# Performance work log

Measured on AMD Instinct MI355X. Metric: run time of the kernel, lower is better.

Reference implementation:

```python
import jax, jax.numpy as jnp
import numpy as np

IN_FEATURES = 256
OUT_FEATURES = 256
GRID_SIZE = 5
SPLINE_ORDER = 3
GRID_LO, GRID_HI = -1.0, 1.0


def _basis_matrix(spline_order):
    # Uniform B-spline basis matrix, replicating calculate_basis_matrix.
    M = np.array([[1.0]], dtype=np.float32)
    scalar = 1.0
    for k in range(2, spline_order + 2):
        t1 = np.pad(M, ((0, 1), (0, 0)))
        t3 = np.pad(M, ((1, 0), (0, 0)))
        t2 = np.zeros((k - 1, k), np.float32)
        t4 = np.zeros((k - 1, k), np.float32)
        for i in range(k - 1):
            t2[i, i] = i + 1
            t2[i, i + 1] = k - (i + 2)
            t4[i, i] = -1.0
            t4[i, i + 1] = 1.0
        M = t1 @ t2 + t3 @ t4
        scalar *= 1.0 / (k - 1)
    return (M * scalar).astype(np.float32)


def setup_inputs() -> dict:
    key = jax.random.key(0)
    kx, kw = jax.random.split(key)
    x = jax.random.uniform(kx, (16384, IN_FEATURES), dtype=jnp.float32)  # in [0,1) within grid range
    weight = jax.random.normal(kw, (IN_FEATURES, OUT_FEATURES, GRID_SIZE + SPLINE_ORDER + 1), dtype=jnp.float32)
    return {"x": x, "weight": weight}


def reference(x, weight):
    s, g = SPLINE_ORDER, GRID_SIZE
    h = (GRID_HI - GRID_LO) / g
    # grid: [-s..g+s] * h + lo, length g + 2s + 1
    grid1d = jnp.arange(-s, g + s + 1, dtype=jnp.float32) * h + GRID_LO

    xi = x[..., None]  # [N, in, 1]
    intervals = (xi >= grid1d[:-1]) & (xi < grid1d[1:])  # [N, in, g+2s]
    idx = jnp.argmax(intervals, axis=-1)  # first true; 0 if none

    # power bases u = [1, u1, u1^2, ..., u1^s]
    floor_val = idx.astype(x.dtype) * h + GRID_LO
    u1 = (x - floor_val) / h  # [N, in]
    u = jnp.stack([jnp.ones_like(u1), u1] + [u1 ** i for i in range(2, s + 1)], axis=-1)  # [N, in, s+1]

    # basis-matrix slice indices (argmax over [zeros | intervals])
    idx2 = jnp.where(intervals.any(-1), idx + 1, 0)  # [N, in]
    floor_idx = (2 * s + g + 1) - idx2  # [N, in]

    B = jnp.asarray(_basis_matrix(s))  # [s+1, s+1]
    B_pad = jnp.pad(B, ((0, 0), (s + g, s + g)))  # [s+1, (s+1)+2(s+g)]
    cols = floor_idx[..., None] + jnp.arange(s + g)  # [N, in, s+g]
    gathered = B_pad[:, cols]  # [s+1, N, in, s+g]

    basis_out = jnp.einsum('nip,pniq->niq', u, gathered)  # [N, in, s+g]
    basis_out = jnp.nan_to_num(basis_out)

    spline_w = weight[:, :, :-1]  # [in, out, s+g]
    base_w = weight[:, :, -1]     # [in, out]
    y = jnp.einsum('niq,ioq->no', basis_out, spline_w) + jnp.einsum('ni,io->no', jax.nn.silu(x), base_w)
    return y
```

## Files before the change

### kernel.cpp

```cpp
#include <hip/hip_runtime.h>
#include <hip/hip_bf16.h>


#define M_TOTAL 16384
#define IF 256
#define OF 256
#define NKT 32
#define THREADS 512

typedef __attribute__((ext_vector_type(8))) __bf16 bf16x8;
typedef __attribute__((ext_vector_type(4))) float f32x4;

__global__ void repack_w(const float* __restrict__ w, __bf16* __restrict__ img) {
    int g = blockIdx.x * 256 + threadIdx.x;
    int lane = g & 63, frag = g >> 6;
    int n  = frag & 3;
    int cg = (frag >> 2) & 3;
    int ks = (frag >> 4) & 1;
    int kt = frag >> 5;
    int col = cg * 64 + n * 16 + (lane & 15);
    int i   = kt * 8 + ks * 4 + (lane >> 4);
    const float s6 = 1.0f / 6.0f;
    bf16x8 v;
#pragma unroll
    for (int c = 0; c < 8; ++c) {
        float f = (c < 6) ? w[(size_t)i * 2304 + col * 9 + c + 2] * s6
                : (c == 6) ? w[(size_t)i * 2304 + col * 9 + 8] : 0.0f;
        v[c] = (__bf16)f;
    }
    ((bf16x8*)img)[g] = v;
}

__device__ __forceinline__ bf16x8 phi_pack(float x) {
    float t  = fmaf(x, 2.5f, 5.5f);
    float fi = floorf(t);
    float u  = (t - fi) - 3.0f;
    float u2 = u * u, u3 = u2 * u;
    float w0 = fmaf(-1.f, u3, fmaf( 3.f, u2, fmaf(-3.f, u, 1.f)));
    float w1 = fmaf( 3.f, u3, fmaf(-6.f, u2, 4.f));
    float w2 = fmaf(-3.f, u3, fmaf( 3.f, u2, fmaf( 3.f, u, 1.f)));
    float w3 = u3;
    bool e1 = fi > 5.5f;
    bool e2 = fi > 6.5f;
    float v0 = e1 ? 0.f : w0;
    float v1 = e2 ? 0.f : (e1 ? w0 : w1);
    float v2 = e2 ? w0  : (e1 ? w1 : w2);
    float v3 = e2 ? w1  : (e1 ? w2 : w3);
    float v4 = e2 ? w2  : (e1 ? w3 : 0.f);
    float v5 = e2 ? w3  : 0.f;
    float sl = x * __builtin_amdgcn_rcpf(1.f + __expf(-x));
    bf16x8 v;
    v[0] = (__bf16)v0; v[1] = (__bf16)v1; v[2] = (__bf16)v2; v[3] = (__bf16)v3;
    v[4] = (__bf16)v4; v[5] = (__bf16)v5; v[6] = (__bf16)sl; v[7] = (__bf16)0.f;
    return v;
}

__device__ __forceinline__ bf16x8 gather_frag(const float* __restrict__ W,
                                              int kt, int col, int ks, int lane) {
    int c2 = col + (lane & 15);
    int i  = kt * 8 + ks * 4 + (lane >> 4);
    const float s6 = 1.0f / 6.0f;
    bf16x8 v;
#pragma unroll
    for (int c = 0; c < 8; ++c) {
        float f = (c < 6) ? W[(size_t)i * 2304 + c2 * 9 + c + 2] * s6
                : (c == 6) ? W[(size_t)i * 2304 + c2 * 9 + 8] : 0.0f;
        v[c] = (__bf16)f;
    }
    return v;
}

template <bool DIRECT_B>
__global__ __launch_bounds__(THREADS, 2)
void kan_gemm(const float* __restrict__ X, const __bf16* __restrict__ Bimg,
              const float* __restrict__ W, float* __restrict__ Y) {
    __shared__ alignas(16) char lds[65536];

    const int tid  = threadIdx.x;
    const int lane = tid & 63;
    const int wv   = tid >> 6;
    const int cg   = wv & 3;
    const int rowg = wv >> 2;
    const int l15  = lane & 15;
    const int l4   = lane >> 4;
    const int brow0 = blockIdx.x * 64;

    const int prow = tid >> 3;
    const int pi   = tid & 7;
    const int pr7  = prow & 7;
    const float* xrow = X + (size_t)(brow0 + prow) * IF;
    const int awbase = prow * 512;

    const int sw    = l15 & 7;
    const int arow0 = rowg * 32 + l15;

    const char* ib = (const char*)Bimg + cg * 4096 + lane * 16;

    f32x4 acc[2][4] = {};
    bf16x8 breg[2][8];
    float xs[4];

#pragma unroll
    for (int w = 0; w < 4; ++w) xs[w] = xrow[w * 8 + pi];
    if (!DIRECT_B) {
#pragma unroll
        for (int ks = 0; ks < 2; ++ks)
#pragma unroll
            for (int n = 0; n < 4; ++n)
                breg[0][ks * 4 + n] = *(const bf16x8*)(ib + ks * 16384 + n * 1024);
    } else {
#pragma unroll
        for (int ks = 0; ks < 2; ++ks)
#pragma unroll
            for (int n = 0; n < 4; ++n)
                breg[0][ks * 4 + n] = gather_frag(W, 0, cg * 64 + n * 16, ks, lane);
    }
#pragma unroll
    for (int w = 0; w < 4; ++w)
        *(bf16x8*)(lds + awbase + (((w * 8 + pi) ^ pr7) << 4)) = phi_pack(xs[w]);
#pragma unroll
    for (int w = 0; w < 4; ++w) xs[w] = xrow[32 + w * 8 + pi];
    __syncthreads();

    for (int c = 0; c < 8; ++c) {
        const char* Ar = lds + ((c & 1) << 15);
        char* Aw = lds + (((c + 1) & 1) << 15);

#pragma unroll
        for (int ktl = 0; ktl < 4; ++ktl) {
            const int kt  = c * 4 + ktl;
            const int ktn = (kt < NKT - 1) ? kt + 1 : kt;

            if (!DIRECT_B) {
                const char* p = ib + (size_t)ktn * 32768;
#pragma unroll
                for (int ks = 0; ks < 2; ++ks)
#pragma unroll
                    for (int n = 0; n < 4; ++n)
                        breg[(ktl + 1) & 1][ks * 4 + n]
                            = *(const bf16x8*)(p + ks * 16384 + n * 1024);
            } else {
#pragma unroll
                for (int ks = 0; ks < 2; ++ks)
#pragma unroll
                    for (int n = 0; n < 4; ++n)
                        breg[(ktl + 1) & 1][ks * 4 + n]
                            = gather_frag(W, ktn, cg * 64 + n * 16, ks, lane);
            }

            bf16x8 aF[2][2];
#pragma unroll
            for (int m = 0; m < 2; ++m)
#pragma unroll
                for (int ks = 0; ks < 2; ++ks)
                    aF[m][ks] = *(const bf16x8*)(Ar + (arow0 + m * 16) * 512
                                    + (((ktl * 8 + ks * 4 + l4) ^ sw) << 4));

            __builtin_amdgcn_s_setprio(1);
#pragma unroll
            for (int ks = 0; ks < 2; ++ks)
#pragma unroll
                for (int m = 0; m < 2; ++m)
#pragma unroll
                    for (int n = 0; n < 4; ++n)
                        acc[m][n] = __builtin_amdgcn_mfma_f32_16x16x32_bf16(
                            aF[m][ks], breg[ktl & 1][ks * 4 + n], acc[m][n], 0, 0, 0);
            __builtin_amdgcn_s_setprio(0);

            if (c < 7) {
                *(bf16x8*)(Aw + awbase + (((ktl * 8 + pi) ^ pr7) << 4))
                    = phi_pack(xs[ktl]);
                if (c < 6) xs[ktl] = xrow[(c + 2) * 32 + ktl * 8 + pi];
            }
        }
        __syncthreads();
    }

#pragma unroll
    for (int m = 0; m < 2; ++m)
#pragma unroll
        for (int n = 0; n < 4; ++n) {
            int col  = cg * 64 + n * 16 + l15;
            int row0 = brow0 + rowg * 32 + m * 16 + l4 * 4;
#pragma unroll
            for (int r = 0; r < 4; ++r)
                Y[(size_t)(row0 + r) * OF + col] = acc[m][n][r];
        }
}

extern "C" void kernel_launch(void* const* d_in, const int* in_sizes, int n_in,
                              void* d_out, int out_size, void* d_ws, size_t ws_size,
                              hipStream_t stream) {
    const float* X = (const float*)d_in[0];
    const float* W = (const float*)d_in[1];
    float* Y = (float*)d_out;

    size_t need = (size_t)65536 * 16;
    dim3 grid(M_TOTAL / 64);

    if (d_ws != nullptr && ws_size >= need) {
        __bf16* img = (__bf16*)d_ws;
        repack_w<<<dim3(256), dim3(256), 0, stream>>>(W, img);
        kan_gemm<false><<<grid, dim3(THREADS), 0, stream>>>(X, img, W, Y);
    } else {
        kan_gemm<true><<<grid, dim3(THREADS), 0, stream>>>(X, nullptr, W, Y);
    }
}
```

Baseline: 36.00 us.

## Split K across wave groups with an LDS reduction instead of splitting rows

The two wave groups in a block now each cover all 64 rows of the block but only half of the reduction dimension, instead of each covering 32 rows over the full K. Each wave therefore holds a 64x64 accumulator tile, and the two partial results are summed through LDS before the store. The goal is to halve the B-fragment loads each wave issues from global memory/L2 and to make better use of each B fragment. In exchange, the LDS buffer doubles to 128KB, which likely limits the kernel to one block per CU, accumulator register pressure doubles, and there is an extra LDS reduction pass at the end. The repack index arithmetic is rewritten but produces the same layout as before.

```diff
diff --git a/kernel.cpp b/kernel.cpp
--- a/kernel.cpp
+++ b/kernel.cpp
@@ -5,7 +5,6 @@
 #define M_TOTAL 16384
 #define IF 256
 #define OF 256
-#define NKT 32
 #define THREADS 512
 
 typedef __attribute__((ext_vector_type(8))) __bf16 bf16x8;
@@ -14,11 +13,11 @@
 __global__ void repack_w(const float* __restrict__ w, __bf16* __restrict__ img) {
     int g = blockIdx.x * 256 + threadIdx.x;
     int lane = g & 63, frag = g >> 6;
-    int n  = frag & 3;
-    int cg = (frag >> 2) & 3;
+    int n  = frag & 1;
+    int wn = (frag >> 1) & 7;
     int ks = (frag >> 4) & 1;
     int kt = frag >> 5;
-    int col = cg * 64 + n * 16 + (lane & 15);
+    int col = wn * 32 + n * 16 + (lane & 15);
     int i   = kt * 8 + ks * 4 + (lane >> 4);
     const float s6 = 1.0f / 6.0f;
     bf16x8 v;
@@ -56,15 +55,15 @@
 }
 
 __device__ __forceinline__ bf16x8 gather_frag(const float* __restrict__ W,
-                                              int kt, int col, int ks, int lane) {
-    int c2 = col + (lane & 15);
-    int i  = kt * 8 + ks * 4 + (lane >> 4);
+                                              int kt, int col16, int ks, int lane) {
+    int col = col16 + (lane & 15);
+    int i   = kt * 8 + ks * 4 + (lane >> 4);
     const float s6 = 1.0f / 6.0f;
     bf16x8 v;
 #pragma unroll
     for (int c = 0; c < 8; ++c) {
-        float f = (c < 6) ? W[(size_t)i * 2304 + c2 * 9 + c + 2] * s6
-                : (c == 6) ? W[(size_t)i * 2304 + c2 * 9 + 8] : 0.0f;
+        float f = (c < 6) ? W[(size_t)i * 2304 + col * 9 + c + 2] * s6
+                : (c == 6) ? W[(size_t)i * 2304 + col * 9 + 8] : 0.0f;
         v[c] = (__bf16)f;
     }
     return v;
@@ -74,13 +73,13 @@
 __global__ __launch_bounds__(THREADS, 2)
 void kan_gemm(const float* __restrict__ X, const __bf16* __restrict__ Bimg,
               const float* __restrict__ W, float* __restrict__ Y) {
-    __shared__ alignas(16) char lds[65536];
+    __shared__ alignas(16) char lds[131072];
 
     const int tid  = threadIdx.x;
     const int lane = tid & 63;
     const int wv   = tid >> 6;
     const int cg   = wv & 3;
-    const int rowg = wv >> 2;
+    const int kg   = wv >> 2;
     const int l15  = lane & 15;
     const int l4   = lane >> 4;
     const int brow0 = blockIdx.x * 64;
@@ -89,50 +88,59 @@
     const int pi   = tid & 7;
     const int pr7  = prow & 7;
     const float* xrow = X + (size_t)(brow0 + prow) * IF;
-    const int awbase = prow * 512;
-
-    const int sw    = l15 & 7;
-    const int arow0 = rowg * 32 + l15;
+    const int awrow = prow * 1024;
+
+    const int sw = l15 & 7;
 
     const char* ib = (const char*)Bimg + cg * 4096 + lane * 16;
-
-    f32x4 acc[2][4] = {};
+    const int kbase = kg * 16;
+
+    f32x4 acc[4][4] = {};
     bf16x8 breg[2][8];
-    float xs[4];
-
-#pragma unroll
-    for (int w = 0; w < 4; ++w) xs[w] = xrow[w * 8 + pi];
+    float xs[8];
+
+#pragma unroll
+    for (int j = 0; j < 4; ++j) {
+        xs[j]     = xrow[pi + j * 8];
+        xs[j + 4] = xrow[128 + pi + j * 8];
+    }
     if (!DIRECT_B) {
+        const char* p = ib + (size_t)kbase * 32768;
 #pragma unroll
         for (int ks = 0; ks < 2; ++ks)
 #pragma unroll
             for (int n = 0; n < 4; ++n)
-                breg[0][ks * 4 + n] = *(const bf16x8*)(ib + ks * 16384 + n * 1024);
+                breg[0][ks * 4 + n] = *(const bf16x8*)(p + ks * 16384 + n * 1024);
     } else {
 #pragma unroll
         for (int ks = 0; ks < 2; ++ks)
 #pragma unroll
             for (int n = 0; n < 4; ++n)
-                breg[0][ks * 4 + n] = gather_frag(W, 0, cg * 64 + n * 16, ks, lane);
-    }
-#pragma unroll
-    for (int w = 0; w < 4; ++w)
-        *(bf16x8*)(lds + awbase + (((w * 8 + pi) ^ pr7) << 4)) = phi_pack(xs[w]);
-#pragma unroll
-    for (int w = 0; w < 4; ++w) xs[w] = xrow[32 + w * 8 + pi];
+                breg[0][ks * 4 + n] = gather_frag(W, kbase, cg * 64 + n * 16, ks, lane);
+    }
+#pragma unroll
+    for (int j = 0; j < 8; ++j) {
+        int u = pi + j * 8;
+        *(bf16x8*)(lds + awrow + ((u ^ pr7) << 4)) = phi_pack(xs[j]);
+    }
+#pragma unroll
+    for (int j = 0; j < 4; ++j) {
+        xs[j]     = xrow[32 + pi + j * 8];
+        xs[j + 4] = xrow[160 + pi + j * 8];
+    }
     __syncthreads();
 
-    for (int c = 0; c < 8; ++c) {
-        const char* Ar = lds + ((c & 1) << 15);
-        char* Aw = lds + (((c + 1) & 1) << 15);
+    for (int cp = 0; cp < 4; ++cp) {
+        const char* Ar = lds + ((cp & 1) << 16);
+        char* Aw = lds + (((cp + 1) & 1) << 16);
 
 #pragma unroll
         for (int ktl = 0; ktl < 4; ++ktl) {
-            const int kt  = c * 4 + ktl;
-            const int ktn = (kt < NKT - 1) ? kt + 1 : kt;
+            const int t  = cp * 4 + ktl;
+            const int tn = (t < 15) ? t + 1 : t;
 
             if (!DIRECT_B) {
-                const char* p = ib + (size_t)ktn * 32768;
+                const char* p = ib + (size_t)(kbase + tn) * 32768;
 #pragma unroll
                 for (int ks = 0; ks < 2; ++ks)
 #pragma unroll
@@ -145,47 +153,64 @@
 #pragma unroll
                     for (int n = 0; n < 4; ++n)
                         breg[(ktl + 1) & 1][ks * 4 + n]
-                            = gather_frag(W, ktn, cg * 64 + n * 16, ks, lane);
-            }
-
-            bf16x8 aF[2][2];
-#pragma unroll
-            for (int m = 0; m < 2; ++m)
-#pragma unroll
-                for (int ks = 0; ks < 2; ++ks)
-                    aF[m][ks] = *(const bf16x8*)(Ar + (arow0 + m * 16) * 512
-                                    + (((ktl * 8 + ks * 4 + l4) ^ sw) << 4));
+                            = gather_frag(W, kbase + tn, cg * 64 + n * 16, ks, lane);
+            }
 
             __builtin_amdgcn_s_setprio(1);
 #pragma unroll
-            for (int ks = 0; ks < 2; ++ks)
-#pragma unroll
-                for (int m = 0; m < 2; ++m)
+            for (int ks = 0; ks < 2; ++ks) {
+                bf16x8 aF[4];
+#pragma unroll
+                for (int m = 0; m < 4; ++m)
+                    aF[m] = *(const bf16x8*)(Ar + (m * 16 + l15) * 1024
+                                + (((kg * 32 + ktl * 8 + ks * 4 + l4) ^ sw) << 4));
+#pragma unroll
+                for (int m = 0; m < 4; ++m)
 #pragma unroll
                     for (int n = 0; n < 4; ++n)
                         acc[m][n] = __builtin_amdgcn_mfma_f32_16x16x32_bf16(
-                            aF[m][ks], breg[ktl & 1][ks * 4 + n], acc[m][n], 0, 0, 0);
+                            aF[m], breg[ktl & 1][ks * 4 + n], acc[m][n], 0, 0, 0);
+            }
             __builtin_amdgcn_s_setprio(0);
 
-            if (c < 7) {
-                *(bf16x8*)(Aw + awbase + (((ktl * 8 + pi) ^ pr7) << 4))
-                    = phi_pack(xs[ktl]);
-                if (c < 6) xs[ktl] = xrow[(c + 2) * 32 + ktl * 8 + pi];
+            if (cp < 3) {
+                int u0 = pi + ktl * 8;
+                int u1 = u0 + 32;
+                *(bf16x8*)(Aw + awrow + ((u0 ^ pr7) << 4)) = phi_pack(xs[ktl]);
+                *(bf16x8*)(Aw + awrow + ((u1 ^ pr7) << 4)) = phi_pack(xs[ktl + 4]);
+                if (cp < 2) {
+                    xs[ktl]     = xrow[(cp + 2) * 32 + pi + ktl * 8];
+                    xs[ktl + 4] = xrow[128 + (cp + 2) * 32 + pi + ktl * 8];
+                }
             }
         }
         __syncthreads();
     }
 
-#pragma unroll
-    for (int m = 0; m < 2; ++m)
-#pragma unroll
-        for (int n = 0; n < 4; ++n) {
-            int col  = cg * 64 + n * 16 + l15;
-            int row0 = brow0 + rowg * 32 + m * 16 + l4 * 4;
-#pragma unroll
-            for (int r = 0; r < 4; ++r)
-                Y[(size_t)(row0 + r) * OF + col] = acc[m][n][r];
-        }
+    if (kg == 1) {
+        char* rb = lds + cg * 16384;
+#pragma unroll
+        for (int m = 0; m < 4; ++m)
+#pragma unroll
+            for (int n = 0; n < 4; ++n)
+                *(f32x4*)(rb + (m * 4 + n) * 1024 + lane * 16) = acc[m][n];
+    }
+    __syncthreads();
+    if (kg == 0) {
+        const char* rb = lds + cg * 16384;
+#pragma unroll
+        for (int m = 0; m < 4; ++m)
+#pragma unroll
+            for (int n = 0; n < 4; ++n) {
+                f32x4 o = *(const f32x4*)(rb + (m * 4 + n) * 1024 + lane * 16);
+                f32x4 s = acc[m][n] + o;
+                int col  = cg * 64 + n * 16 + l15;
+                int row0 = brow0 + m * 16 + l4 * 4;
+#pragma unroll
+                for (int r = 0; r < 4; ++r)
+                    Y[(size_t)(row0 + r) * OF + col] = s[r];
+            }
+    }
 }
 
 extern "C" void kernel_launch(void* const* d_in, const int* in_sizes, int n_in,
```

After: 30.40 us. -15.6%, faster.
